# Kernel tuning notes

Measured on AMD Instinct MI355X. Metric: run time of the kernel, lower is better.

Reference implementation:

```python
import jax, jax.numpy as jnp
import numpy as np

B, S, DM, DC = 16, 4096, 1280, 768
N_AOE, N_IMG, N_DELTA = 16, 16, 16
ANAT_GATE, DIS_GATE, DELTA_SCALE = 0.5, 0.5, 1.0


def setup_inputs() -> dict:
    key = jax.random.key(0)
    ks = jax.random.split(key, 9)
    def lin(k, fan_in, fan_out):
        return jax.random.normal(k, (fan_in, fan_out), jnp.float32) / np.sqrt(fan_in)
    return {
        "hidden_states": jax.random.normal(ks[0], (B, S, DM), jnp.float32),
        "encoder_hidden_states": jax.random.normal(ks[1], (B, N_AOE + N_IMG + N_DELTA, DC), jnp.float32),
        "w_q": lin(ks[2], DM, DM),
        "w_k": lin(ks[3], DC, DM),
        "w_v": lin(ks[4], DC, DM),
        "w_k_dis": lin(ks[5], DC, DM),
        "w_v_dis": lin(ks[6], DC, DM),
        "w_out": lin(ks[7], DM, DM),
        "b_out": jnp.zeros((DM,), jnp.float32),
        "n_heads": 8,
    }


def _heads(x, h):
    b, s, d = x.shape
    return x.reshape(b, s, h, d // h).transpose(0, 2, 1, 3)  # [B,H,S,dh]


def _attend(q, k, v, scale):
    # q:[B,H,Sq,dh], k/v:[B,H,Sk,dh], Sk small (16)
    scores = jnp.einsum("bhqd,bhkd->bhqk", q, k) * scale
    probs = jax.nn.softmax(scores, axis=-1)
    return jnp.einsum("bhqk,bhkd->bhqd", probs, v)


def reference(hidden_states, encoder_hidden_states, w_q, w_k, w_v,
              w_k_dis, w_v_dis, w_out, b_out, n_heads):
    residual = hidden_states
    dh = DM // n_heads
    scale = 1.0 / np.sqrt(dh)

    dis_tok = encoder_hidden_states[:, :N_AOE, :]
    anat_tok = encoder_hidden_states[:, N_AOE:N_AOE + N_IMG, :]
    delta_tok = encoder_hidden_states[:, -N_DELTA:, :]

    q = _heads(hidden_states @ w_q, n_heads)
    z_anat = _attend(q, _heads(anat_tok @ w_k, n_heads), _heads(anat_tok @ w_v, n_heads), scale)
    z_dis = _attend(q, _heads(dis_tok @ w_k_dis, n_heads), _heads(dis_tok @ w_v_dis, n_heads), scale)
    z_delta = _attend(q, _heads(delta_tok @ w_k_dis, n_heads), _heads(delta_tok @ w_v_dis, n_heads), scale)

    z = ANAT_GATE * z_anat + DIS_GATE * z_dis + DELTA_SCALE * z_delta
    out = z.transpose(0, 2, 1, 3).reshape(hidden_states.shape[0], -1, DM)
    out = out @ w_out + b_out  # to_out[0]; to_out[1] dropout = identity in eval
    return out + residual  # residual_connection, rescale_output_factor=1.0
```

## Files before the change

kernel.cpp:

```cpp
#include <hip/hip_runtime.h>
#include <hip/hip_bf16.h>

#define B_ 16
#define S_ 4096
#define DM_ 1280
#define DC_ 768
#define NC_ 384
#define SCALE_ 0.07905694150420949f

typedef __attribute__((ext_vector_type(8))) short bf16x8;
typedef __attribute__((ext_vector_type(4))) float f32x4;
typedef __attribute__((ext_vector_type(4))) unsigned short u16x4;

#define S_BARRIER() asm volatile("s_barrier" ::: "memory")
#define WAIT_VM(n) asm volatile("s_waitcnt vmcnt(" #n ")" ::: "memory")
#define WAIT_LGKM0() asm volatile("s_waitcnt lgkmcnt(0)" ::: "memory")

__device__ __forceinline__ unsigned short f2bf(float f) {
    unsigned int u = __builtin_bit_cast(unsigned int, f);
    u = (u + 0x7FFFu + ((u >> 16) & 1u)) >> 16;
    return (unsigned short)u;
}

__device__ __forceinline__ bf16x8 pack8(float4 x0, float4 x1) {
    bf16x8 a;
    a[0] = __builtin_bit_cast(short, __float2bfloat16(x0.x));
    a[1] = __builtin_bit_cast(short, __float2bfloat16(x0.y));
    a[2] = __builtin_bit_cast(short, __float2bfloat16(x0.z));
    a[3] = __builtin_bit_cast(short, __float2bfloat16(x0.w));
    a[4] = __builtin_bit_cast(short, __float2bfloat16(x1.x));
    a[5] = __builtin_bit_cast(short, __float2bfloat16(x1.y));
    a[6] = __builtin_bit_cast(short, __float2bfloat16(x1.z));
    a[7] = __builtin_bit_cast(short, __float2bfloat16(x1.w));
    return a;
}

__device__ __forceinline__ void gload16(const void* g, void* l) {
    __builtin_amdgcn_global_load_lds(
        (const __attribute__((address_space(1))) void*)g,
        (__attribute__((address_space(3))) void*)l, 16, 0, 0);
}

__device__ __forceinline__ void tcvt_body(const float* __restrict__ in,
                                          unsigned short* __restrict__ out,
                                          int R, int C, int bx, int by, int tid) {
    __shared__ float tile[32][33];
    int c0 = bx * 32, r0 = by * 32;
    int tx = tid & 31, ty = tid >> 5;
    for (int i = ty; i < 32; i += 8)
        tile[i][tx] = in[(size_t)(r0 + i) * C + c0 + tx];
    __syncthreads();
    for (int i = ty; i < 32; i += 8)
        out[(size_t)(c0 + i) * R + r0 + tx] = f2bf(tile[tx][i]);
}

__global__ __launch_bounds__(256)
void k_prep(const float* __restrict__ wq, const float* __restrict__ wk,
            const float* __restrict__ wv, const float* __restrict__ wkd,
            const float* __restrict__ wvd, const float* __restrict__ wout,
            unsigned short* __restrict__ wq_bf, unsigned short* __restrict__ wTk,
            unsigned short* __restrict__ wTv, unsigned short* __restrict__ wTkd,
            unsigned short* __restrict__ wTvd, unsigned short* __restrict__ woutT) {
    int bid = blockIdx.x, tid = threadIdx.x;
    if (bid < 1600) {
        int i = bid * 256 + tid;
        float4 v = ((const float4*)wq)[i];
        u16x4 o = { f2bf(v.x), f2bf(v.y), f2bf(v.z), f2bf(v.w) };
        ((u16x4*)wq_bf)[i] = o;
    } else if (bid < 2560) {
        int r = bid - 1600; tcvt_body(wk,  wTk,  DC_, DM_, r % 40, r / 40, tid);
    } else if (bid < 3520) {
        int r = bid - 2560; tcvt_body(wv,  wTv,  DC_, DM_, r % 40, r / 40, tid);
    } else if (bid < 4480) {
        int r = bid - 3520; tcvt_body(wkd, wTkd, DC_, DM_, r % 40, r / 40, tid);
    } else if (bid < 5440) {
        int r = bid - 4480; tcvt_body(wvd, wTvd, DC_, DM_, r % 40, r / 40, tid);
    } else {
        int r = bid - 5440; tcvt_body(wout, woutT, DM_, DM_, r % 40, r / 40, tid);
    }
}

__global__ __launch_bounds__(256)
void k_projM(const float* __restrict__ enc,
             const unsigned short* __restrict__ wTk, const unsigned short* __restrict__ wTv,
             const unsigned short* __restrict__ wTkd, const unsigned short* __restrict__ wTvd,
             unsigned short* __restrict__ KV) {
    int bid = blockIdx.x;
    int j = bid / 80, rem = bid % 80, b = rem / 5, nt = rem % 5;
    int tid = threadIdx.x, w = tid >> 6, l = tid & 63, l15 = l & 15, l4 = l >> 4;
    int tok0 = (j < 2) ? 16 : ((j < 4) ? 0 : 32);
    const unsigned short* wT = (j == 0) ? wTk : (j == 1) ? wTv : (j == 2 || j == 4) ? wTkd : wTvd;
    const float* ap = enc + ((size_t)(b * 48 + tok0 + l15)) * DC_;
    f32x4 zero = {0.f, 0.f, 0.f, 0.f};
    f32x4 acc[4];
    #pragma unroll
    for (int t = 0; t < 4; t++) acc[t] = zero;
    for (int kk = 0; kk < 24; kk++) {
        const float4* hp = (const float4*)(ap + kk * 32 + l4 * 8);
        bf16x8 af = pack8(hp[0], hp[1]);
        #pragma unroll
        for (int t = 0; t < 4; t++) {
            int n0 = nt * 256 + w * 64 + t * 16;
            bf16x8 bf = *(const bf16x8*)(wT + (size_t)(n0 + l15) * DC_ + kk * 32 + l4 * 8);
            acc[t] = __builtin_amdgcn_mfma_f32_16x16x32_bf16(af, bf, acc[t], 0, 0, 0);
        }
    }
    #pragma unroll
    for (int t = 0; t < 4; t++) {
        int e = nt * 256 + w * 64 + t * 16 + l15;
        #pragma unroll
        for (int r = 0; r < 4; r++)
            KV[((size_t)(j * 16 + b) * 16 + l4 * 4 + r) * DM_ + e] = f2bf(acc[t][r]);
    }
}

__global__ __launch_bounds__(256)
void k_au(const unsigned short* __restrict__ KV, const unsigned short* __restrict__ wqbf,
          const unsigned short* __restrict__ woutT,
          unsigned short* __restrict__ At2, unsigned short* __restrict__ Ut2) {
    int bid0 = blockIdx.x;
    bool isA = bid0 < 384;
    int bid = isA ? bid0 : bid0 - 384;
    int b = bid & 15, r_ = bid >> 4, x = r_ >> 3, h = r_ & 7;
    int tid = threadIdx.x, w = tid >> 6, l = tid & 63, l15 = l & 15, l4 = l >> 4;
    int xh = x * 8 + h;
    int jrow = isA ? (2 * x) : (2 * x + 1);
    const unsigned short* wmat = isA ? wqbf : woutT;
    float postscale = isA ? SCALE_ : ((x == 2) ? 1.0f : 0.5f);
    bf16x8 bfr[5];
    #pragma unroll
    for (int kk = 0; kk < 5; kk++)
        bfr[kk] = *(const bf16x8*)(KV + ((size_t)(jrow * 16 + b) * 16 + l15) * DM_ + h * 160 + kk * 32 + l4 * 8);
    f32x4 zero = {0.f, 0.f, 0.f, 0.f};
    for (int tt = 0; tt < 20; tt++) {
        int d0 = w * 320 + tt * 16;
        f32x4 acc = zero;
        if (isA) {
            #pragma unroll
            for (int kk = 0; kk < 5; kk++) {
                bf16x8 af = *(const bf16x8*)(wmat + (size_t)(d0 + l15) * DM_ + h * 160 + kk * 32 + l4 * 8);
                acc = __builtin_amdgcn_mfma_f32_16x16x32_bf16(af, bfr[kk], acc, 0, 0, 0);
            }
            int c = xh * 16 + l15;
            u16x4 pk;
            #pragma unroll
            for (int r = 0; r < 4; r++) pk[r] = f2bf(acc[r] * postscale);
            *(u16x4*)(At2 + ((size_t)(b * 40 + (d0 >> 5)) * NC_ + c) * 32 + (d0 & 31) + l4 * 4) = pk;
        } else {
            #pragma unroll
            for (int kk = 0; kk < 5; kk++) {
                bf16x8 af = *(const bf16x8*)(wmat + (size_t)(d0 + l15) * DM_ + h * 160 + kk * 32 + l4 * 8);
                acc = __builtin_amdgcn_mfma_f32_16x16x32_bf16(bfr[kk], af, acc, 0, 0, 0);
            }
            int e = d0 + l15;
            u16x4 pk;
            #pragma unroll
            for (int r = 0; r < 4; r++) pk[r] = f2bf(acc[r] * postscale);
            *(u16x4*)(Ut2 + ((size_t)(b * 12 + (xh >> 1)) * DM_ + e) * 32 + (xh & 1) * 16 + l4 * 4) = pk;
        }
    }
}

__global__ __launch_bounds__(256, 2)
void k_scores7(const float* __restrict__ hid, const unsigned short* __restrict__ At2,
               unsigned short* __restrict__ P2) {
    __shared__ char smem[73728];
    unsigned short* Apnl = (unsigned short*)smem;
    char* Hlds = smem + 49152;
    int bid = blockIdx.x;
    int orig = (bid & 7) * 128 + (bid >> 3);
    int b = orig >> 6, st = orig & 63;
    int s0 = st * 64;
    int tid = threadIdx.x, w = tid >> 6, l = tid & 63, l15 = l & 15, l4 = l >> 4;
    int rdsw = (l4 ^ ((l15 >> 1) & 3)) * 8;
    const unsigned short* Ab = At2 + (size_t)b * 40 * NC_ * 32;
    const float* hsrc = hid + ((size_t)b * S_ + s0) * DM_;
    f32x4 zero = {0.f, 0.f, 0.f, 0.f};
    f32x4 acc[4][6];
    #pragma unroll
    for (int si = 0; si < 4; si++)
        #pragma unroll
        for (int cj = 0; cj < 6; cj++) acc[si][cj] = zero;

    auto stageA = [&](int kk, int ab) {
        const unsigned short* slab = Ab + (size_t)kk * (NC_ * 32);
        #pragma unroll
        for (int i = 0; i < 6; i++) {
            int idx = i * 256 + tid;
            int c = idx >> 2, m = (idx & 3) ^ ((c >> 1) & 3);
            gload16(slab + (size_t)c * 32 + m * 8, smem + ab * 24576 + idx * 16);
        }
    };
    auto stageH = [&](int kk, int hb) {
        #pragma unroll
        for (int i = 0; i < 2; i++) {
            int idx = i * 256 + tid;
            int r = idx >> 3, sg = (idx & 7) ^ (r & 7);
            gload16(hsrc + (size_t)r * DM_ + kk * 32 + sg * 4, Hlds + hb * 8192 + idx * 16);
        }
    };
    auto compute = [&](int ab, int hb) {
        bf16x8 hpk[4];
        #pragma unroll
        for (int si = 0; si < 4; si++) {
            int r = si * 16 + l15;
            float4 lo = *(const float4*)(Hlds + hb * 8192 + r * 128 + (((2 * l4) ^ (l15 & 7)) * 16));
            float4 hi = *(const float4*)(Hlds + hb * 8192 + r * 128 + (((2 * l4 + 1) ^ (l15 & 7)) * 16));
            hpk[si] = pack8(lo, hi);
        }
        __builtin_amdgcn_s_setprio(1);
        #pragma unroll
        for (int cj = 0; cj < 6; cj++) {
            bf16x8 af = *(const bf16x8*)&Apnl[ab * 12288 + (w * 96 + cj * 16 + l15) * 32 + rdsw];
            #pragma unroll
            for (int si = 0; si < 4; si++)
                acc[si][cj] = __builtin_amdgcn_mfma_f32_16x16x32_bf16(af, hpk[si], acc[si][cj], 0, 0, 0);
        }
        __builtin_amdgcn_s_setprio(0);
    };
    auto SITER = [&](int kk) {
        stageA(kk + 1, (kk + 1) & 1);
        stageH(kk + 2, (kk + 2) % 3);
        WAIT_VM(10);
        S_BARRIER();
        compute(kk & 1, kk % 3);
        WAIT_LGKM0();
        S_BARRIER();
    };

    stageA(0, 0); stageH(0, 0); stageH(1, 1);
    for (int k0 = 0; k0 < 36; k0 += 6) {
        SITER(k0 + 0); SITER(k0 + 1); SITER(k0 + 2);
        SITER(k0 + 3); SITER(k0 + 4); SITER(k0 + 5);
    }
    SITER(36); SITER(37);
    stageA(39, 1);
    WAIT_VM(8);
    S_BARRIER();
    compute(0, 38 % 3);
    WAIT_LGKM0();
    S_BARRIER();
    WAIT_VM(0);
    S_BARRIER();
    compute(1, 39 % 3);
    WAIT_LGKM0();
    S_BARRIER();

    #pragma unroll
    for (int si = 0; si < 4; si++) {
        int s_l = si * 16 + l15;
        #pragma unroll
        for (int cj = 0; cj < 6; cj++) {
            float v0 = acc[si][cj][0], v1 = acc[si][cj][1], v2 = acc[si][cj][2], v3 = acc[si][cj][3];
            float mx = fmaxf(fmaxf(v0, v1), fmaxf(v2, v3));
            mx = fmaxf(mx, __shfl_xor(mx, 16));
            mx = fmaxf(mx, __shfl_xor(mx, 32));
            float e0 = __expf(v0 - mx), e1 = __expf(v1 - mx), e2 = __expf(v2 - mx), e3 = __expf(v3 - mx);
            float sm = e0 + e1 + e2 + e3;
            sm += __shfl_xor(sm, 16);
            sm += __shfl_xor(sm, 32);
            float rs = 1.0f / sm;
            u16x4 pk = { f2bf(e0 * rs), f2bf(e1 * rs), f2bf(e2 * rs), f2bf(e3 * rs) };
            int c = w * 96 + cj * 16 + l4 * 4;
            int chunk = ((c & 31) >> 3) ^ (s_l & 3);
            *(u16x4*)(smem + (c >> 5) * 4096 + s_l * 64 + chunk * 16 + (l4 & 1) * 8) = pk;
        }
    }
    __syncthreads();

    unsigned short* P2b = P2 + (size_t)b * 12 * S_ * 32;
    #pragma unroll
    for (int i = 0; i < 12; i++) {
        int sl = tid >> 2, m = tid & 3;
        uint4 v = *(const uint4*)(smem + i * 4096 + sl * 64 + ((m ^ (sl & 3)) * 16));
        *(uint4*)(P2b + ((size_t)i * S_ + s0 + sl) * 32 + m * 8) = v;
    }
}

__global__ __launch_bounds__(256, 2)
void k_pv5(const unsigned short* __restrict__ P2, const unsigned short* __restrict__ Ut2,
           const float* __restrict__ hid, const float* __restrict__ bo,
           float* __restrict__ out) {
    __shared__ unsigned short Plds[2][2][4096];
    __shared__ unsigned short Ulds[2][2][4096];
    int bid = blockIdx.x;
    int orig = (bid & 7) * 640 + (bid >> 3);
    int b = orig / 320, rem = orig % 320;
    int st = rem / 10, ec = rem % 10;
    int s0 = st * 128, e0 = ec * 128;
    int tid = threadIdx.x, w = tid >> 6, l = tid & 63, l15 = l & 15, l4 = l >> 4;
    int wr = w >> 1, wc = w & 1;
    int rdsw = (l4 ^ ((l15 >> 1) & 3)) * 8;
    const unsigned short* Pb = P2 + (size_t)b * 12 * S_ * 32;
    const unsigned short* Ub = Ut2 + (size_t)b * 12 * DM_ * 32;
    f32x4 zero = {0.f, 0.f, 0.f, 0.f};
    f32x4 acc[4][4];
    #pragma unroll
    for (int si = 0; si < 4; si++)
        #pragma unroll
        for (int ej = 0; ej < 4; ej++) acc[si][ej] = zero;

    auto stage = [&](int kk2, int buf) {
        #pragma unroll
        for (int sub = 0; sub < 2; sub++) {
            int kk = kk2 * 2 + sub;
            const unsigned short* Pslab = Pb + (size_t)kk * S_ * 32;
            const unsigned short* Uslab = Ub + (size_t)kk * DM_ * 32;
            #pragma unroll
            for (int i = 0; i < 2; i++) {
                int idx = i * 256 + tid;
                int r = idx >> 2, m = (idx & 3) ^ ((r >> 1) & 3);
                gload16(Pslab + ((size_t)s0 + r) * 32 + m * 8, (char*)&Plds[buf][sub][0] + idx * 16);
                gload16(Uslab + ((size_t)e0 + r) * 32 + m * 8, (char*)&Ulds[buf][sub][0] + idx * 16);
            }
        }
    };
    auto compute = [&](int buf) {
        #pragma unroll
        for (int sub = 0; sub < 2; sub++) {
            bf16x8 uf[4], pf[4];
            #pragma unroll
            for (int ej = 0; ej < 4; ej++)
                uf[ej] = *(const bf16x8*)&Ulds[buf][sub][(wr * 64 + ej * 16 + l15) * 32 + rdsw];
            #pragma unroll
            for (int si = 0; si < 4; si++)
                pf[si] = *(const bf16x8*)&Plds[buf][sub][(wc * 64 + si * 16 + l15) * 32 + rdsw];
            __builtin_amdgcn_s_setprio(1);
            #pragma unroll
            for (int si = 0; si < 4; si++)
                #pragma unroll
                for (int ej = 0; ej < 4; ej++)
                    acc[si][ej] = __builtin_amdgcn_mfma_f32_16x16x32_bf16(uf[ej], pf[si], acc[si][ej], 0, 0, 0);
            __builtin_amdgcn_s_setprio(0);
        }
    };

    stage(0, 0);
    for (int kk2 = 0; kk2 < 5; kk2++) {
        stage(kk2 + 1, (kk2 + 1) & 1);
        WAIT_VM(8);
        S_BARRIER();
        compute(kk2 & 1);
        WAIT_LGKM0();
        S_BARRIER();
    }
    WAIT_VM(0);
    S_BARRIER();
    compute(1);

    float4 b4[4];
    #pragma unroll
    for (int ej = 0; ej < 4; ej++)
        b4[ej] = *(const float4*)(bo + e0 + wr * 64 + ej * 16 + l4 * 4);
    #pragma unroll
    for (int si = 0; si < 4; si++) {
        int srow = s0 + wc * 64 + si * 16 + l15;
        #pragma unroll
        for (int ej = 0; ej < 4; ej++) {
            int ecol = e0 + wr * 64 + ej * 16 + l4 * 4;
            size_t off = ((size_t)b * S_ + srow) * DM_ + ecol;
            float4 h4 = *(const float4*)(hid + off);
            f32x4 a = acc[si][ej];
            float4 o4;
            o4.x = a[0] + b4[ej].x + h4.x;
            o4.y = a[1] + b4[ej].y + h4.y;
            o4.z = a[2] + b4[ej].z + h4.z;
            o4.w = a[3] + b4[ej].w + h4.w;
            *(float4*)(out + off) = o4;
        }
    }
}

extern "C" void kernel_launch(void* const* d_in, const int* in_sizes, int n_in,
                              void* d_out, int out_size, void* d_ws, size_t ws_size,
                              hipStream_t stream) {
    const float* hid  = (const float*)d_in[0];
    const float* enc  = (const float*)d_in[1];
    const float* wq   = (const float*)d_in[2];
    const float* wk   = (const float*)d_in[3];
    const float* wv   = (const float*)d_in[4];
    const float* wkd  = (const float*)d_in[5];
    const float* wvd  = (const float*)d_in[6];
    const float* wout = (const float*)d_in[7];
    const float* bo   = (const float*)d_in[8];
    float* out = (float*)d_out;

    char* ws = (char*)d_ws;
    unsigned short* At2    = (unsigned short*)(ws);
    unsigned short* Ut2    = (unsigned short*)(ws + 15728640);
    unsigned short* KV     = (unsigned short*)(ws + 31457280);
    unsigned short* wq_bf  = (unsigned short*)(ws + 35389440);
    unsigned short* woutT  = (unsigned short*)(ws + 38666240);
    unsigned short* wTk    = (unsigned short*)(ws + 41943040);
    unsigned short* wTv    = (unsigned short*)(ws + 43909120);
    unsigned short* wTkd   = (unsigned short*)(ws + 45875200);
    unsigned short* wTvd   = (unsigned short*)(ws + 47841280);
    unsigned short* P2     = (unsigned short*)(ws + 35389440);

    k_prep<<<7040, 256, 0, stream>>>(wq, wk, wv, wkd, wvd, wout,
                                     wq_bf, wTk, wTv, wTkd, wTvd, woutT);
    k_projM<<<480, 256, 0, stream>>>(enc, wTk, wTv, wTkd, wTvd, KV);
    k_au<<<768, 256, 0, stream>>>(KV, wq_bf, woutT, At2, Ut2);
    k_scores7<<<1024, 256, 0, stream>>>(hid, At2, P2);
    k_pv5<<<5120, 256, 0, stream>>>(P2, Ut2, hid, bo, out);
}
```

Before: 405.0 us.

## Fuse scores-softmax and PV output kernels, keeping probabilities in LDS

Merges the scores/softmax kernel and the PV+output-projection kernel into one kernel. The softmax probabilities stay in shared memory and are consumed directly by a loop over five 256-wide output column chunks. This removes the global write and re-read of the probability buffer and one kernel launch. In exchange, each block does more serial work, re-streams the U panel per block, and uses more LDS.

```diff
diff --git a/kernel.cpp b/kernel.cpp
--- a/kernel.cpp
+++ b/kernel.cpp
@@ -162,11 +162,13 @@
 }
 
 __global__ __launch_bounds__(256, 2)
-void k_scores7(const float* __restrict__ hid, const unsigned short* __restrict__ At2,
-               unsigned short* __restrict__ P2) {
-    __shared__ char smem[73728];
+void k_fused(const float* __restrict__ hid, const unsigned short* __restrict__ At2,
+             const unsigned short* __restrict__ Ut2, const float* __restrict__ bo,
+             float* __restrict__ out) {
+    __shared__ char smem[81920];
     unsigned short* Apnl = (unsigned short*)smem;
     char* Hlds = smem + 49152;
+    unsigned short* Ulds2 = (unsigned short*)(smem + 49152);
     int bid = blockIdx.x;
     int orig = (bid & 7) * 128 + (bid >> 3);
     int b = orig >> 6, st = orig & 63;
@@ -176,197 +178,166 @@
     const unsigned short* Ab = At2 + (size_t)b * 40 * NC_ * 32;
     const float* hsrc = hid + ((size_t)b * S_ + s0) * DM_;
     f32x4 zero = {0.f, 0.f, 0.f, 0.f};
-    f32x4 acc[4][6];
-    #pragma unroll
-    for (int si = 0; si < 4; si++)
-        #pragma unroll
-        for (int cj = 0; cj < 6; cj++) acc[si][cj] = zero;
-
-    auto stageA = [&](int kk, int ab) {
-        const unsigned short* slab = Ab + (size_t)kk * (NC_ * 32);
-        #pragma unroll
-        for (int i = 0; i < 6; i++) {
-            int idx = i * 256 + tid;
-            int c = idx >> 2, m = (idx & 3) ^ ((c >> 1) & 3);
-            gload16(slab + (size_t)c * 32 + m * 8, smem + ab * 24576 + idx * 16);
-        }
-    };
-    auto stageH = [&](int kk, int hb) {
-        #pragma unroll
-        for (int i = 0; i < 2; i++) {
-            int idx = i * 256 + tid;
-            int r = idx >> 3, sg = (idx & 7) ^ (r & 7);
-            gload16(hsrc + (size_t)r * DM_ + kk * 32 + sg * 4, Hlds + hb * 8192 + idx * 16);
-        }
-    };
-    auto compute = [&](int ab, int hb) {
-        bf16x8 hpk[4];
-        #pragma unroll
-        for (int si = 0; si < 4; si++) {
-            int r = si * 16 + l15;
-            float4 lo = *(const float4*)(Hlds + hb * 8192 + r * 128 + (((2 * l4) ^ (l15 & 7)) * 16));
-            float4 hi = *(const float4*)(Hlds + hb * 8192 + r * 128 + (((2 * l4 + 1) ^ (l15 & 7)) * 16));
-            hpk[si] = pack8(lo, hi);
-        }
-        __builtin_amdgcn_s_setprio(1);
-        #pragma unroll
-        for (int cj = 0; cj < 6; cj++) {
-            bf16x8 af = *(const bf16x8*)&Apnl[ab * 12288 + (w * 96 + cj * 16 + l15) * 32 + rdsw];
-            #pragma unroll
-            for (int si = 0; si < 4; si++)
-                acc[si][cj] = __builtin_amdgcn_mfma_f32_16x16x32_bf16(af, hpk[si], acc[si][cj], 0, 0, 0);
-        }
-        __builtin_amdgcn_s_setprio(0);
-    };
-    auto SITER = [&](int kk) {
-        stageA(kk + 1, (kk + 1) & 1);
-        stageH(kk + 2, (kk + 2) % 3);
-        WAIT_VM(10);
+
+    {
+        f32x4 acc[4][6];
+        #pragma unroll
+        for (int si = 0; si < 4; si++)
+            #pragma unroll
+            for (int cj = 0; cj < 6; cj++) acc[si][cj] = zero;
+
+        auto stageA = [&](int kk, int ab) {
+            const unsigned short* slab = Ab + (size_t)kk * (NC_ * 32);
+            #pragma unroll
+            for (int i = 0; i < 6; i++) {
+                int idx = i * 256 + tid;
+                int c = idx >> 2, m = (idx & 3) ^ ((c >> 1) & 3);
+                gload16(slab + (size_t)c * 32 + m * 8, smem + ab * 24576 + idx * 16);
+            }
+        };
+        auto stageH = [&](int kk, int hb) {
+            #pragma unroll
+            for (int i = 0; i < 2; i++) {
+                int idx = i * 256 + tid;
+                int r = idx >> 3, sg = (idx & 7) ^ (r & 7);
+                gload16(hsrc + (size_t)r * DM_ + kk * 32 + sg * 4, Hlds + hb * 8192 + idx * 16);
+            }
+        };
+        auto compute = [&](int ab, int hb) {
+            bf16x8 hpk[4];
+            #pragma unroll
+            for (int si = 0; si < 4; si++) {
+                int r = si * 16 + l15;
+                float4 lo = *(const float4*)(Hlds + hb * 8192 + r * 128 + (((2 * l4) ^ (l15 & 7)) * 16));
+                float4 hi = *(const float4*)(Hlds + hb * 8192 + r * 128 + (((2 * l4 + 1) ^ (l15 & 7)) * 16));
+                hpk[si] = pack8(lo, hi);
+            }
+            __builtin_amdgcn_s_setprio(1);
+            #pragma unroll
+            for (int cj = 0; cj < 6; cj++) {
+                bf16x8 af = *(const bf16x8*)&Apnl[ab * 12288 + (w * 96 + cj * 16 + l15) * 32 + rdsw];
+                #pragma unroll
+                for (int si = 0; si < 4; si++)
+                    acc[si][cj] = __builtin_amdgcn_mfma_f32_16x16x32_bf16(af, hpk[si], acc[si][cj], 0, 0, 0);
+            }
+            __builtin_amdgcn_s_setprio(0);
+        };
+        auto SITER = [&](int kk) {
+            stageA(kk + 1, (kk + 1) & 1);
+            stageH(kk + 2, (kk + 2) % 3);
+            WAIT_VM(10);
+            S_BARRIER();
+            compute(kk & 1, kk % 3);
+            WAIT_LGKM0();
+            S_BARRIER();
+        };
+
+        stageA(0, 0); stageH(0, 0); stageH(1, 1);
+        for (int k0 = 0; k0 < 36; k0 += 6) {
+            SITER(k0 + 0); SITER(k0 + 1); SITER(k0 + 2);
+            SITER(k0 + 3); SITER(k0 + 4); SITER(k0 + 5);
+        }
+        SITER(36); SITER(37);
+        stageA(39, 1);
+        WAIT_VM(8);
         S_BARRIER();
-        compute(kk & 1, kk % 3);
+        compute(0, 38 % 3);
         WAIT_LGKM0();
         S_BARRIER();
+        WAIT_VM(0);
+        S_BARRIER();
+        compute(1, 39 % 3);
+        WAIT_LGKM0();
+        S_BARRIER();
+
+        #pragma unroll
+        for (int si = 0; si < 4; si++) {
+            int s_l = si * 16 + l15;
+            #pragma unroll
+            for (int cj = 0; cj < 6; cj++) {
+                float v0 = acc[si][cj][0], v1 = acc[si][cj][1], v2 = acc[si][cj][2], v3 = acc[si][cj][3];
+                float mx = fmaxf(fmaxf(v0, v1), fmaxf(v2, v3));
+                mx = fmaxf(mx, __shfl_xor(mx, 16));
+                mx = fmaxf(mx, __shfl_xor(mx, 32));
+                float e0 = __expf(v0 - mx), e1 = __expf(v1 - mx), e2 = __expf(v2 - mx), e3 = __expf(v3 - mx);
+                float sm = e0 + e1 + e2 + e3;
+                sm += __shfl_xor(sm, 16);
+                sm += __shfl_xor(sm, 32);
+                float rs = 1.0f / sm;
+                u16x4 pk = { f2bf(e0 * rs), f2bf(e1 * rs), f2bf(e2 * rs), f2bf(e3 * rs) };
+                int c = w * 96 + cj * 16 + l4 * 4;
+                int chunk = ((c & 31) >> 3) ^ (s_l & 3);
+                *(u16x4*)(smem + (c >> 5) * 4096 + s_l * 64 + chunk * 16 + (l4 & 1) * 8) = pk;
+            }
+        }
+    }
+    __syncthreads();
+
+    const unsigned short* Ub = Ut2 + (size_t)b * 12 * DM_ * 32;
+    auto stageU = [&](int kk2, int ec, int buf) {
+        const unsigned short* slab = Ub + ((size_t)kk2 * DM_ + ec * 256) * 32;
+        #pragma unroll
+        for (int i = 0; i < 4; i++) {
+            int idx = i * 256 + tid;
+            int r = idx >> 2, m = (idx & 3) ^ ((r >> 1) & 3);
+            gload16(slab + (size_t)r * 32 + m * 8, (char*)Ulds2 + buf * 16384 + idx * 16);
+        }
     };
 
-    stageA(0, 0); stageH(0, 0); stageH(1, 1);
-    for (int k0 = 0; k0 < 36; k0 += 6) {
-        SITER(k0 + 0); SITER(k0 + 1); SITER(k0 + 2);
-        SITER(k0 + 3); SITER(k0 + 4); SITER(k0 + 5);
-    }
-    SITER(36); SITER(37);
-    stageA(39, 1);
-    WAIT_VM(8);
-    S_BARRIER();
-    compute(0, 38 % 3);
-    WAIT_LGKM0();
-    S_BARRIER();
-    WAIT_VM(0);
-    S_BARRIER();
-    compute(1, 39 % 3);
-    WAIT_LGKM0();
-    S_BARRIER();
-
-    #pragma unroll
-    for (int si = 0; si < 4; si++) {
-        int s_l = si * 16 + l15;
-        #pragma unroll
-        for (int cj = 0; cj < 6; cj++) {
-            float v0 = acc[si][cj][0], v1 = acc[si][cj][1], v2 = acc[si][cj][2], v3 = acc[si][cj][3];
-            float mx = fmaxf(fmaxf(v0, v1), fmaxf(v2, v3));
-            mx = fmaxf(mx, __shfl_xor(mx, 16));
-            mx = fmaxf(mx, __shfl_xor(mx, 32));
-            float e0 = __expf(v0 - mx), e1 = __expf(v1 - mx), e2 = __expf(v2 - mx), e3 = __expf(v3 - mx);
-            float sm = e0 + e1 + e2 + e3;
-            sm += __shfl_xor(sm, 16);
-            sm += __shfl_xor(sm, 32);
-            float rs = 1.0f / sm;
-            u16x4 pk = { f2bf(e0 * rs), f2bf(e1 * rs), f2bf(e2 * rs), f2bf(e3 * rs) };
-            int c = w * 96 + cj * 16 + l4 * 4;
-            int chunk = ((c & 31) >> 3) ^ (s_l & 3);
-            *(u16x4*)(smem + (c >> 5) * 4096 + s_l * 64 + chunk * 16 + (l4 & 1) * 8) = pk;
-        }
-    }
-    __syncthreads();
-
-    unsigned short* P2b = P2 + (size_t)b * 12 * S_ * 32;
-    #pragma unroll
-    for (int i = 0; i < 12; i++) {
-        int sl = tid >> 2, m = tid & 3;
-        uint4 v = *(const uint4*)(smem + i * 4096 + sl * 64 + ((m ^ (sl & 3)) * 16));
-        *(uint4*)(P2b + ((size_t)i * S_ + s0 + sl) * 32 + m * 8) = v;
-    }
-}
-
-__global__ __launch_bounds__(256, 2)
-void k_pv5(const unsigned short* __restrict__ P2, const unsigned short* __restrict__ Ut2,
-           const float* __restrict__ hid, const float* __restrict__ bo,
-           float* __restrict__ out) {
-    __shared__ unsigned short Plds[2][2][4096];
-    __shared__ unsigned short Ulds[2][2][4096];
-    int bid = blockIdx.x;
-    int orig = (bid & 7) * 640 + (bid >> 3);
-    int b = orig / 320, rem = orig % 320;
-    int st = rem / 10, ec = rem % 10;
-    int s0 = st * 128, e0 = ec * 128;
-    int tid = threadIdx.x, w = tid >> 6, l = tid & 63, l15 = l & 15, l4 = l >> 4;
-    int wr = w >> 1, wc = w & 1;
-    int rdsw = (l4 ^ ((l15 >> 1) & 3)) * 8;
-    const unsigned short* Pb = P2 + (size_t)b * 12 * S_ * 32;
-    const unsigned short* Ub = Ut2 + (size_t)b * 12 * DM_ * 32;
-    f32x4 zero = {0.f, 0.f, 0.f, 0.f};
-    f32x4 acc[4][4];
-    #pragma unroll
-    for (int si = 0; si < 4; si++)
-        #pragma unroll
-        for (int ej = 0; ej < 4; ej++) acc[si][ej] = zero;
-
-    auto stage = [&](int kk2, int buf) {
-        #pragma unroll
-        for (int sub = 0; sub < 2; sub++) {
-            int kk = kk2 * 2 + sub;
-            const unsigned short* Pslab = Pb + (size_t)kk * S_ * 32;
-            const unsigned short* Uslab = Ub + (size_t)kk * DM_ * 32;
-            #pragma unroll
-            for (int i = 0; i < 2; i++) {
-                int idx = i * 256 + tid;
-                int r = idx >> 2, m = (idx & 3) ^ ((r >> 1) & 3);
-                gload16(Pslab + ((size_t)s0 + r) * 32 + m * 8, (char*)&Plds[buf][sub][0] + idx * 16);
-                gload16(Uslab + ((size_t)e0 + r) * 32 + m * 8, (char*)&Ulds[buf][sub][0] + idx * 16);
-            }
-        }
-    };
-    auto compute = [&](int buf) {
-        #pragma unroll
-        for (int sub = 0; sub < 2; sub++) {
+    for (int ec = 0; ec < 5; ec++) {
+        f32x4 accp[4][4];
+        #pragma unroll
+        for (int si = 0; si < 4; si++)
+            #pragma unroll
+            for (int ej = 0; ej < 4; ej++) accp[si][ej] = zero;
+
+        stageU(0, ec, 0);
+        for (int kk2 = 0; kk2 < 12; kk2++) {
+            if (kk2 < 11) {
+                stageU(kk2 + 1, ec, (kk2 + 1) & 1);
+                WAIT_VM(4);
+            } else {
+                WAIT_VM(0);
+            }
+            S_BARRIER();
+            int buf = kk2 & 1;
             bf16x8 uf[4], pf[4];
             #pragma unroll
             for (int ej = 0; ej < 4; ej++)
-                uf[ej] = *(const bf16x8*)&Ulds[buf][sub][(wr * 64 + ej * 16 + l15) * 32 + rdsw];
-            #pragma unroll
-            for (int si = 0; si < 4; si++)
-                pf[si] = *(const bf16x8*)&Plds[buf][sub][(wc * 64 + si * 16 + l15) * 32 + rdsw];
+                uf[ej] = *(const bf16x8*)&Ulds2[buf * 8192 + (w * 64 + ej * 16 + l15) * 32 + rdsw];
+            #pragma unroll
+            for (int si = 0; si < 4; si++) {
+                int s_l = si * 16 + l15;
+                pf[si] = *(const bf16x8*)(smem + kk2 * 4096 + s_l * 64 + ((l4 ^ (l15 & 3)) * 16));
+            }
             __builtin_amdgcn_s_setprio(1);
             #pragma unroll
             for (int si = 0; si < 4; si++)
                 #pragma unroll
                 for (int ej = 0; ej < 4; ej++)
-                    acc[si][ej] = __builtin_amdgcn_mfma_f32_16x16x32_bf16(uf[ej], pf[si], acc[si][ej], 0, 0, 0);
+                    accp[si][ej] = __builtin_amdgcn_mfma_f32_16x16x32_bf16(uf[ej], pf[si], accp[si][ej], 0, 0, 0);
             __builtin_amdgcn_s_setprio(0);
-        }
-    };
-
-    stage(0, 0);
-    for (int kk2 = 0; kk2 < 5; kk2++) {
-        stage(kk2 + 1, (kk2 + 1) & 1);
-        WAIT_VM(8);
-        S_BARRIER();
-        compute(kk2 & 1);
-        WAIT_LGKM0();
-        S_BARRIER();
-    }
-    WAIT_VM(0);
-    S_BARRIER();
-    compute(1);
-
-    float4 b4[4];
-    #pragma unroll
-    for (int ej = 0; ej < 4; ej++)
-        b4[ej] = *(const float4*)(bo + e0 + wr * 64 + ej * 16 + l4 * 4);
-    #pragma unroll
-    for (int si = 0; si < 4; si++) {
-        int srow = s0 + wc * 64 + si * 16 + l15;
+            WAIT_LGKM0();
+            S_BARRIER();
+        }
+
         #pragma unroll
         for (int ej = 0; ej < 4; ej++) {
-            int ecol = e0 + wr * 64 + ej * 16 + l4 * 4;
-            size_t off = ((size_t)b * S_ + srow) * DM_ + ecol;
-            float4 h4 = *(const float4*)(hid + off);
-            f32x4 a = acc[si][ej];
-            float4 o4;
-            o4.x = a[0] + b4[ej].x + h4.x;
-            o4.y = a[1] + b4[ej].y + h4.y;
-            o4.z = a[2] + b4[ej].z + h4.z;
-            o4.w = a[3] + b4[ej].w + h4.w;
-            *(float4*)(out + off) = o4;
+            int e0c = ec * 256 + w * 64 + ej * 16 + l4 * 4;
+            float4 b4 = *(const float4*)(bo + e0c);
+            #pragma unroll
+            for (int si = 0; si < 4; si++) {
+                int srow = s0 + si * 16 + l15;
+                size_t off = ((size_t)b * S_ + srow) * DM_ + e0c;
+                float4 h4 = *(const float4*)(hid + off);
+                f32x4 a = accp[si][ej];
+                float4 o4;
+                o4.x = a[0] + b4.x + h4.x;
+                o4.y = a[1] + b4.y + h4.y;
+                o4.z = a[2] + b4.z + h4.z;
+                o4.w = a[3] + b4.w + h4.w;
+                *(float4*)(out + off) = o4;
+            }
         }
     }
 }
@@ -395,12 +366,10 @@
     unsigned short* wTv    = (unsigned short*)(ws + 43909120);
     unsigned short* wTkd   = (unsigned short*)(ws + 45875200);
     unsigned short* wTvd   = (unsigned short*)(ws + 47841280);
-    unsigned short* P2     = (unsigned short*)(ws + 35389440);
 
     k_prep<<<7040, 256, 0, stream>>>(wq, wk, wv, wkd, wvd, wout,
                                      wq_bf, wTk, wTv, wTkd, wTvd, woutT);
     k_projM<<<480, 256, 0, stream>>>(enc, wTk, wTv, wTkd, wTvd, KV);
     k_au<<<768, 256, 0, stream>>>(KV, wq_bf, woutT, At2, Ut2);
-    k_scores7<<<1024, 256, 0, stream>>>(hid, At2, P2);
-    k_pv5<<<5120, 256, 0, stream>>>(P2, Ut2, hid, bo, out);
-}
+    k_fused<<<1024, 256, 0, stream>>>(hid, At2, Ut2, bo, out);
+}
```

Result: faster. 393.8 us (-2.8%).
